# Kernel optimization log

Hardware: AMD Instinct MI355X
Metric: run time of the kernel (lower is better)

The kernel has to match this reference:

```python
import jax, jax.numpy as jnp
import numpy as np

CONV_CH, FRAG_DIM, N_P, N_T, PROJ = 32, 8, 6, 12, 64
B, T, W = 64, 256, 20


def _p(key, shape, scale=0.05):
    return (jax.random.normal(key, shape, dtype=jnp.float32) * scale)


def setup_inputs() -> dict:
    key = jax.random.key(0)
    ks = jax.random.split(key, 24)
    inp = {
        'pressure': jax.random.normal(ks[0], (B, T, W, N_P), dtype=jnp.float32),
        'torque': jax.random.normal(ks[1], (B, T, W, N_T), dtype=jnp.float32),
        'fragility': jax.random.uniform(ks[2], (B, 1), dtype=jnp.float32),
        # pressure encoder conv weights (O, I, K)
        'pw1': _p(ks[3], (CONV_CH, N_P, 3)), 'pb1': _p(ks[4], (CONV_CH,)),
        'pw2': _p(ks[5], (CONV_CH, CONV_CH, 3)), 'pb2': _p(ks[6], (CONV_CH,)),
        # torque encoder
        'tw1': _p(ks[7], (CONV_CH, N_T, 3)), 'tb1': _p(ks[8], (CONV_CH,)),
        'tw2': _p(ks[9], (CONV_CH, CONV_CH, 3)), 'tb2': _p(ks[10], (CONV_CH,)),
        # fragility Linear(1, 8)
        'fw': _p(ks[11], (FRAG_DIM, 1)), 'fb': _p(ks[12], (FRAG_DIM,)),
        # project Linear(72, 64)
        'prw': _p(ks[13], (PROJ, 2 * CONV_CH + FRAG_DIM)), 'prb': _p(ks[14], (PROJ,)),
        # LSTM (torch gate order i,f,g,o)
        'Wih': _p(ks[15], (4 * PROJ, PROJ)), 'Whh': _p(ks[16], (4 * PROJ, PROJ)),
        'bih': _p(ks[17], (4 * PROJ,)), 'bhh': _p(ks[18], (4 * PROJ,)),
        # head Linear(64, 4)
        'hw': _p(ks[19], (4, PROJ)), 'hb': _p(ks[20], (4,)),
    }
    return inp


def _conv1d(x, w, b):
    # x: (N, C, L), w: (O, I, K) -> (N, O, L-K+1), valid padding
    y = jax.lax.conv_general_dilated(x, w, (1,), 'VALID',
                                     dimension_numbers=('NCH', 'OIH', 'NCH'))
    return y + b[None, :, None]


def _encoder(x, w1, b1, w2, b2):
    # x: (N, C, L); conv-relu-conv-relu-global avg pool -> (N, CONV_CH)
    h = jax.nn.relu(_conv1d(x, w1, b1))
    h = jax.nn.relu(_conv1d(h, w2, b2))
    return jnp.mean(h, axis=-1)


def _lstm(x, Wih, Whh, bih, bhh):
    # x: (B, T, H); torch LSTM, gates i,f,g,o
    Bq, Tq, H = x.shape
    bias = bih + bhh
    xg = jnp.einsum('bth,gh->btg', x, Wih) + bias  # precompute input gates

    def step(carry, gt):
        h, c = carry
        g = gt + h @ Whh.T
        i, f, gg, o = jnp.split(g, 4, axis=-1)
        c = jax.nn.sigmoid(f) * c + jax.nn.sigmoid(i) * jnp.tanh(gg)
        h = jax.nn.sigmoid(o) * jnp.tanh(c)
        return (h, c), h

    init = (jnp.zeros((Bq, H), x.dtype), jnp.zeros((Bq, H), x.dtype))
    (hT, cT), hs = jax.lax.scan(step, init, xg.transpose(1, 0, 2))
    return hs.transpose(1, 0, 2), hT, cT


def reference(pressure, torque, fragility,
              pw1, pb1, pw2, pb2, tw1, tb1, tw2, tb2,
              fw, fb, prw, prb, Wih, Whh, bih, bhh, hw, hb):
    Bq, Tq = pressure.shape[:2]
    # batch all T windows at once: (B*T, C, L)
    p = pressure.reshape(Bq * Tq, W, N_P).transpose(0, 2, 1)
    t = torque.reshape(Bq * Tq, W, N_T).transpose(0, 2, 1)
    pf = _encoder(p, pw1, pb1, pw2, pb2)                    # (B*T, 32)
    tf = _encoder(t, tw1, tb1, tw2, tb2)                    # (B*T, 32)
    ff = jax.nn.relu(fragility @ fw.T + fb)                 # (B, 8)
    ff = jnp.broadcast_to(ff[:, None, :], (Bq, Tq, FRAG_DIM)).reshape(Bq * Tq, FRAG_DIM)
    cat = jnp.concatenate([pf, tf, ff], axis=1)             # (B*T, 72)
    feat = jax.nn.relu(cat @ prw.T + prb).reshape(Bq, Tq, PROJ)
    lstm_out, hT, cT = _lstm(feat, Wih, Whh, bih, bhh)
    out = jax.nn.sigmoid(lstm_out @ hw.T + hb)              # (B, T, 4)
    return out, hT, cT
```

## Files before the change

### kernel.cpp

```cpp
#include <hip/hip_runtime.h>
#include <math.h>

#define B_   64
#define T_   256
#define W_   20
#define NP_  6
#define NT_  12
#define CC_  32
#define FD_  8
#define PR_  64

#define LOG2E  1.4426950408889634f

typedef float v2f __attribute__((ext_vector_type(2)));
typedef _Float16 half2_t __attribute__((ext_vector_type(2)));

#define PINU(x) asm volatile("" : "+v"(x))
#define WAVE_SYNC() asm volatile("s_waitcnt lgkmcnt(0)" ::: "memory")

#define H2(u) __builtin_bit_cast(half2_t, (u))
#define EXP2N(x) __builtin_amdgcn_exp2f(x)


__device__ __forceinline__ unsigned packh2(float a, float b) {
    union { _Float16 h[2]; unsigned u; } cv;
    cv.h[0] = (_Float16)a; cv.h[1] = (_Float16)b;
    return cv.u;
}

__device__ __forceinline__ float sigmoidf_(float x) {
    return __builtin_amdgcn_rcpf(1.0f + EXP2N(-LOG2E * x));
}

#define W1PT_N  (18 * 64)
#define W2G_N   (64 * 48)
#define PRWT_N  (18 * 64 * 4)
#define WIHT_N  (16 * 4 * 64 * 4)
#define BSUM_N  256
#define PREP_TOTAL (W1PT_N + W2G_N + PRWT_N + WIHT_N + BSUM_N)

__global__ void prep_kernel(
    const float* __restrict__ pw1, const float* __restrict__ tw1,
    const float* __restrict__ pw2, const float* __restrict__ tw2,
    const float* __restrict__ prw, const float* __restrict__ Wih,
    const float* __restrict__ bih, const float* __restrict__ bhh,
    unsigned* __restrict__ w1pT, unsigned* __restrict__ w2g,
    float* __restrict__ prwT4, float* __restrict__ wihT4,
    float* __restrict__ bsum)
{
    int id = blockIdx.x * 256 + threadIdx.x;
    if (id < W1PT_N) {
        int lane = id & 63, m3 = id >> 6;
        int s = lane >> 5, o = lane & 31;
        int m = m3 / 3, k = m3 - 3 * m;
        unsigned v;
        if (s == 0)
            v = (m < 3) ? packh2(pw1[o * 18 + (2 * m) * 3 + k],
                                 pw1[o * 18 + (2 * m + 1) * 3 + k]) : 0u;
        else
            v = packh2(tw1[o * 36 + (2 * m) * 3 + k],
                       tw1[o * 36 + (2 * m + 1) * 3 + k]);
        w1pT[id] = v;
        return;
    }
    id -= W1PT_N;
    if (id < W2G_N) {
        int r = id / 48, c = id - 48 * r;
        int s = r >> 5, o = r & 31;
        int m = c / 3, k = c - 3 * m;
        const float* src = s ? tw2 : pw2;
        w2g[id] = packh2(src[o * 96 + (2 * m) * 3 + k],
                         src[o * 96 + (2 * m + 1) * 3 + k]);
        return;
    }
    id -= W2G_N;
    if (id < PRWT_N) {
        int j = id & 3, t = id >> 2;
        int lane = t & 63, kq = t >> 6;
        prwT4[id] = prw[lane * 72 + kq * 4 + j];
        return;
    }
    id -= PRWT_N;
    if (id < WIHT_N) {
        int j = id & 3, t = id >> 2;
        int lane = t & 63, gg = t >> 6;
        int gi = gg & 3, kq = gg >> 2;
        wihT4[id] = Wih[(gi * 64 + lane) * 64 + kq * 4 + j];
        return;
    }
    id -= WIHT_N;
    if (id < BSUM_N) bsum[id] = bih[id] + bhh[id];
}

__global__ __launch_bounds__(256, 4) void encoder_kernel(
    const float* __restrict__ pressure, const float* __restrict__ torque,
    const float* __restrict__ frag,
    const float* __restrict__ pb1, const float* __restrict__ tb1,
    const float* __restrict__ pb2, const float* __restrict__ tb2,
    const float* __restrict__ fw,  const float* __restrict__ fb,
    const float* __restrict__ prb,
    const unsigned* __restrict__ w1pT, const unsigned* __restrict__ w2g,
    const float* __restrict__ prwT4, const float* __restrict__ wihT4,
    const float* __restrict__ bsum,
    float* __restrict__ xg)
{
    const int tid  = threadIdx.x;
    const int wv   = tid >> 6;
    const int lane = tid & 63;
    const int bt   = blockIdx.x * 4 + wv;
    const int b    = bt >> 8;
    const int  o   = lane & 31;
    const bool isp = lane < 32;
    const int  s   = isp ? 0 : 1;

    __shared__ unsigned w2p[64 * 49];
    __shared__ __align__(16) unsigned xwp[4][2][120];
    __shared__ __align__(16) unsigned h1p[4][2][320];
    __shared__ __align__(16) float catb4[4][72];
    __shared__ __align__(16) float featsh4[4][64];

    float* catb   = catb4[wv];
    float* featsh = featsh4[wv];

    for (int idx = tid; idx < 64 * 48; idx += 256) {
        int r = idx / 48, c = idx - r * 48;
        w2p[r * 49 + c] = w2g[idx];
    }

    {
        unsigned* xz = &xwp[wv][0][0];
        #pragma unroll
        for (int idx = lane; idx < 240; idx += 64) xz[idx] = 0;
    }
    const float* pin = pressure + (size_t)bt * (W_ * NP_);
    for (int idx = lane; idx < W_ * NP_; idx += 64) {
        int w = idx / NP_, i = idx - w * NP_;
        ((_Float16*)&xwp[wv][0][(i >> 1) * 20 + w])[i & 1] = (_Float16)pin[idx];
    }
    const float* tin = torque + (size_t)bt * (W_ * NT_);
    for (int idx = lane; idx < W_ * NT_; idx += 64) {
        int w = idx / NT_, i = idx - w * NT_;
        ((_Float16*)&xwp[wv][1][(i >> 1) * 20 + w])[i & 1] = (_Float16)tin[idx];
    }
    if (lane < FD_) catb[64 + lane] = fmaxf(frag[b] * fw[lane] + fb[lane], 0.0f);

    unsigned w1p[18];
    #pragma unroll
    for (int m3 = 0; m3 < 18; ++m3) w1p[m3] = w1pT[m3 * 64 + lane];

    const float bz1 = isp ? pb1[o] : tb1[o];
    const float bz2 = isp ? pb2[o] : tb2[o];
    WAVE_SYNC();

    {
        const unsigned* xr = &xwp[wv][s][0];
        float acc[18];
        #pragma unroll
        for (int l = 0; l < 18; ++l) acc[l] = bz1;
        #pragma unroll
        for (int m = 0; m < 6; ++m) {
            uint4 r4[5];
            const uint4* rp = (const uint4*)(xr + m * 20);
            #pragma unroll
            for (int q = 0; q < 5; ++q) r4[q] = rp[q];
            const unsigned* rw = (const unsigned*)r4;
            const half2_t wk0 = H2(w1p[m * 3]), wk1 = H2(w1p[m * 3 + 1]), wk2 = H2(w1p[m * 3 + 2]);
            #pragma unroll
            for (int l = 0; l < 18; ++l) {
                float a = acc[l];
                a = __builtin_amdgcn_fdot2(wk0, H2(rw[l]),     a, false);
                a = __builtin_amdgcn_fdot2(wk1, H2(rw[l + 1]), a, false);
                a = __builtin_amdgcn_fdot2(wk2, H2(rw[l + 2]), a, false);
                acc[l] = a;
            }
        }
        #pragma unroll
        for (int l = 0; l < 18; ++l)
            ((_Float16*)&h1p[wv][s][(o >> 1) * 20 + l])[o & 1] = (_Float16)fmaxf(acc[l], 0.0f);
    }
    __syncthreads();

    {
        const unsigned* hr   = &h1p[wv][s][0];
        const unsigned* wrow = w2p + lane * 49;
        float sacc[16];
        #pragma unroll
        for (int l = 0; l < 16; ++l) sacc[l] = bz2;
        #pragma unroll 4
        for (int m = 0; m < 16; ++m) {
            uint4 r4[5];
            const uint4* rp = (const uint4*)(hr + m * 20);
            #pragma unroll
            for (int q = 0; q < 5; ++q) r4[q] = rp[q];
            const unsigned* rw = (const unsigned*)r4;
            const half2_t wk0 = H2(wrow[m * 3]), wk1 = H2(wrow[m * 3 + 1]), wk2 = H2(wrow[m * 3 + 2]);
            #pragma unroll
            for (int l = 0; l < 16; ++l) {
                float a = sacc[l];
                a = __builtin_amdgcn_fdot2(wk0, H2(rw[l]),     a, false);
                a = __builtin_amdgcn_fdot2(wk1, H2(rw[l + 1]), a, false);
                a = __builtin_amdgcn_fdot2(wk2, H2(rw[l + 2]), a, false);
                sacc[l] = a;
            }
        }
        float m2 = 0.0f;
        #pragma unroll
        for (int l = 0; l < 16; ++l) m2 += fmaxf(sacc[l], 0.0f);
        catb[lane] = m2 * 0.0625f;
    }
    WAVE_SYNC();

    {
        float acc = prb[lane];
        const float4* w4 = (const float4*)prwT4;
        const float4* c4 = (const float4*)catb;
        #pragma unroll
        for (int q = 0; q < 18; ++q) {
            float4 w = w4[q * 64 + lane];
            float4 cv = c4[q];
            acc += w.x * cv.x + w.y * cv.y + w.z * cv.z + w.w * cv.w;
        }
        featsh[lane] = fmaxf(acc, 0.0f);
    }
    WAVE_SYNC();

    {
        float4 fr[16];
        const float4* f4 = (const float4*)featsh;
        #pragma unroll
        for (int q = 0; q < 16; ++q) fr[q] = f4[q];
        float* xgrow = xg + (size_t)bt * 256;
        const float4* w44 = (const float4*)wihT4;
        #pragma unroll
        for (int gi = 0; gi < 4; ++gi) {
            float acc = bsum[gi * 64 + lane];
            #pragma unroll
            for (int q = 0; q < 16; ++q) {
                float4 w = w44[(q * 4 + gi) * 64 + lane];
                acc += w.x * fr[q].x + w.y * fr[q].y + w.z * fr[q].z + w.w * fr[q].w;
            }
            xgrow[gi * 64 + lane] = acc;
        }
    }
}

__global__ __launch_bounds__(64, 1) void lstm_kernel(
    const float* __restrict__ xg,
    const float* __restrict__ Whh,
    float* __restrict__ hout,
    float* __restrict__ dout)
{
    const int b = blockIdx.x;
    const int j = threadIdx.x;

    __shared__ __align__(16) _Float16 hs[64];

    unsigned wi[32], wf[32], wg[32], wo[32];
    {
        const v2f* ri = (const v2f*)(Whh + (size_t)(j)       * 64);
        const v2f* rf = (const v2f*)(Whh + (size_t)(64  + j) * 64);
        const v2f* rg = (const v2f*)(Whh + (size_t)(128 + j) * 64);
        const v2f* ro = (const v2f*)(Whh + (size_t)(192 + j) * 64);
        #pragma unroll
        for (int q = 0; q < 32; ++q) {
            v2f w;
            w = ri[q]; wi[q] = packh2(w.x, w.y);
            w = rf[q]; wf[q] = packh2(w.x, w.y);
            w = rg[q]; wg[q] = packh2(w.x, w.y);
            w = ro[q]; wo[q] = packh2(w.x, w.y);
        }
        #pragma unroll
        for (int q = 0; q < 32; ++q) { PINU(wi[q]); PINU(wf[q]); PINU(wg[q]); PINU(wo[q]); }
    }

    const float* xp = xg + (size_t)b * T_ * 256 + j;
    float4* hq4 = (float4*)(hout + (size_t)b * T_ * 64);

    float c = 0.0f;
    float h = 0.0f;
    hs[j] = (_Float16)0.0f;
    WAVE_SYNC();

    float xc0 = xp[0],   xc1 = xp[64],  xc2 = xp[128], xc3 = xp[192];
    float xn0 = xp[256], xn1 = xp[320], xn2 = xp[384], xn3 = xp[448];

    for (int tq = 0; tq < T_ / 4; ++tq) {
        float4 hacc;
        #pragma unroll
        for (int k = 0; k < 4; ++k) {
            const int t = tq * 4 + k;
            const int tp = (t + 2) * 256;
            float xf0 = xp[tp], xf1 = xp[tp + 64], xf2 = xp[tp + 128], xf3 = xp[tp + 192];

            uint4 hb[8];
            const uint4* hp = (const uint4*)hs;
            #pragma unroll
            for (int q = 0; q < 8; ++q) hb[q] = hp[q];
            const unsigned* hu = (const unsigned*)hb;

            float ai0 = xc0, af0 = xc1, ag0 = xc2, ao0 = xc3;
            float ai1 = 0.0f, af1 = 0.0f, ag1 = 0.0f, ao1 = 0.0f;
            #pragma unroll
            for (int q = 0; q < 32; q += 2) {
                half2_t h0 = H2(hu[q]), h1 = H2(hu[q + 1]);
                ai0 = __builtin_amdgcn_fdot2(H2(wi[q]),     h0, ai0, false);
                af0 = __builtin_amdgcn_fdot2(H2(wf[q]),     h0, af0, false);
                ag0 = __builtin_amdgcn_fdot2(H2(wg[q]),     h0, ag0, false);
                ao0 = __builtin_amdgcn_fdot2(H2(wo[q]),     h0, ao0, false);
                ai1 = __builtin_amdgcn_fdot2(H2(wi[q + 1]), h1, ai1, false);
                af1 = __builtin_amdgcn_fdot2(H2(wf[q + 1]), h1, af1, false);
                ag1 = __builtin_amdgcn_fdot2(H2(wg[q + 1]), h1, ag1, false);
                ao1 = __builtin_amdgcn_fdot2(H2(wo[q + 1]), h1, ao1, false);
            }
            const float ai = ai0 + ai1, af = af0 + af1;
            const float ag = ag0 + ag1, ao = ao0 + ao1;

            const float I = __builtin_amdgcn_rcpf(1.0f + EXP2N(-LOG2E * ai));
            const float F = __builtin_amdgcn_rcpf(1.0f + EXP2N(-LOG2E * af));
            const float O = __builtin_amdgcn_rcpf(1.0f + EXP2N(-LOG2E * ao));
            const float rgv = __builtin_amdgcn_rcpf(1.0f + EXP2N((2.0f * LOG2E) * ag));
            const float IG  = __builtin_fmaf(-(I + I), rgv, I);
            c = __builtin_fmaf(F, c, IG);
            const float rcv = __builtin_amdgcn_rcpf(1.0f + EXP2N((2.0f * LOG2E) * c));
            h = __builtin_fmaf(-(O + O), rcv, O);

            hs[j] = (_Float16)h;
            (&hacc.x)[k] = h;

            xc0 = xn0; xc1 = xn1; xc2 = xn2; xc3 = xn3;
            xn0 = xf0; xn1 = xf1; xn2 = xf2; xn3 = xf3;
        }
        hq4[tq * 64 + j] = hacc;
    }

    dout[B_ * T_ * 4 + b * 64 + j]           = h;
    dout[B_ * T_ * 4 + B_ * 64 + b * 64 + j] = c;
}

__global__ __launch_bounds__(256) void head_kernel(
    const float* __restrict__ hout, const float* __restrict__ hw,
    const float* __restrict__ hb, float* __restrict__ out)
{
    const int blk = blockIdx.x;
    const int tid = threadIdx.x;

    __shared__ __align__(16) float hsh[64 * 68];
    __shared__ __align__(16) float wsh[256];
    __shared__ float bsh[4];

    const float4* s4 = (const float4*)(hout + (size_t)blk * 64 * 64);
    for (int q = tid; q < 1024; q += 256) {
        int tqL = q >> 6;
        int j   = q & 63;
        float4 v = s4[q];
        #pragma unroll
        for (int k = 0; k < 4; ++k)
            hsh[(tqL * 4 + k) * 68 + j] = (&v.x)[k];
    }
    if (tid < 64) ((float4*)wsh)[tid] = ((const float4*)hw)[tid];
    if (tid < 4)  bsh[tid] = hb[tid];
    __syncthreads();

    const int r = tid >> 2, m = tid & 3;
    const float4* hv = (const float4*)(hsh + r * 68);
    const float4* wv = (const float4*)(wsh + m * 64);
    float acc = bsh[m];
    #pragma unroll
    for (int q = 0; q < 16; ++q) {
        float4 a = hv[q], w = wv[q];
        acc += a.x * w.x + a.y * w.y + a.z * w.z + a.w * w.w;
    }
    out[(size_t)blk * 256 + tid] = sigmoidf_(acc);
}

extern "C" void kernel_launch(void* const* d_in, const int* in_sizes, int n_in,
                              void* d_out, int out_size, void* d_ws, size_t ws_size,
                              hipStream_t stream) {
    const float* pressure = (const float*)d_in[0];
    const float* torque   = (const float*)d_in[1];
    const float* frag     = (const float*)d_in[2];
    const float* pw1 = (const float*)d_in[3];
    const float* pb1 = (const float*)d_in[4];
    const float* pw2 = (const float*)d_in[5];
    const float* pb2 = (const float*)d_in[6];
    const float* tw1 = (const float*)d_in[7];
    const float* tb1 = (const float*)d_in[8];
    const float* tw2 = (const float*)d_in[9];
    const float* tb2 = (const float*)d_in[10];
    const float* fw  = (const float*)d_in[11];
    const float* fb  = (const float*)d_in[12];
    const float* prw = (const float*)d_in[13];
    const float* prb = (const float*)d_in[14];
    const float* Wih = (const float*)d_in[15];
    const float* Whh = (const float*)d_in[16];
    const float* bih = (const float*)d_in[17];
    const float* bhh = (const float*)d_in[18];
    const float* hw  = (const float*)d_in[19];
    const float* hb  = (const float*)d_in[20];

    float* out = (float*)d_out;

    float* xg   = (float*)d_ws;
    float* hout = xg + (size_t)B_ * T_ * 256;

    unsigned* w1pT = (unsigned*)hout;
    unsigned* w2g  = w1pT + W1PT_N;
    float*   prwT4 = (float*)(w2g + W2G_N);
    float*   wihT4 = prwT4 + PRWT_N;
    float*   bsumP = wihT4 + WIHT_N;

    prep_kernel<<<(PREP_TOTAL + 255) / 256, 256, 0, stream>>>(
        pw1, tw1, pw2, tw2, prw, Wih, bih, bhh,
        w1pT, w2g, prwT4, wihT4, bsumP);

    encoder_kernel<<<B_ * T_ / 4, 256, 0, stream>>>(
        pressure, torque, frag,
        pb1, tb1, pb2, tb2, fw, fb, prb,
        w1pT, w2g, prwT4, wihT4, bsumP, xg);

    lstm_kernel<<<B_, 64, 0, stream>>>(xg, Whh, hout, out);

    head_kernel<<<B_ * T_ / 64, 256, 0, stream>>>(hout, hw, hb, out);
}
```

Baseline: 196.1 us.

## Fuse encoder and LSTM into one persistent kernel with per-chunk ready flags

```diff
diff --git a/kernel.cpp b/kernel.cpp
--- a/kernel.cpp
+++ b/kernel.cpp
@@ -39,15 +39,21 @@
 #define BSUM_N  256
 #define PREP_TOTAL (W1PT_N + W2G_N + PRWT_N + WIHT_N + BSUM_N)
 
+__device__ unsigned g_w1pT[W1PT_N];
+__device__ unsigned g_w2g[W2G_N];
+__device__ float    g_prwT4[PRWT_N];
+__device__ float    g_wihT4[WIHT_N];
+__device__ float    g_bsum[BSUM_N];
+__device__ unsigned long long g_ready[B_];
+
 __global__ void prep_kernel(
     const float* __restrict__ pw1, const float* __restrict__ tw1,
     const float* __restrict__ pw2, const float* __restrict__ tw2,
     const float* __restrict__ prw, const float* __restrict__ Wih,
-    const float* __restrict__ bih, const float* __restrict__ bhh,
-    unsigned* __restrict__ w1pT, unsigned* __restrict__ w2g,
-    float* __restrict__ prwT4, float* __restrict__ wihT4,
-    float* __restrict__ bsum)
+    const float* __restrict__ bih, const float* __restrict__ bhh)
 {
+    if (blockIdx.x == 0 && threadIdx.x < B_) g_ready[threadIdx.x] = 0ull;
+
     int id = blockIdx.x * 256 + threadIdx.x;
     if (id < W1PT_N) {
         int lane = id & 63, m3 = id >> 6;
@@ -60,7 +66,7 @@
         else
             v = packh2(tw1[o * 36 + (2 * m) * 3 + k],
                        tw1[o * 36 + (2 * m + 1) * 3 + k]);
-        w1pT[id] = v;
+        g_w1pT[id] = v;
         return;
     }
     id -= W1PT_N;
@@ -69,15 +75,15 @@
         int s = r >> 5, o = r & 31;
         int m = c / 3, k = c - 3 * m;
         const float* src = s ? tw2 : pw2;
-        w2g[id] = packh2(src[o * 96 + (2 * m) * 3 + k],
-                         src[o * 96 + (2 * m + 1) * 3 + k]);
+        g_w2g[id] = packh2(src[o * 96 + (2 * m) * 3 + k],
+                           src[o * 96 + (2 * m + 1) * 3 + k]);
         return;
     }
     id -= W2G_N;
     if (id < PRWT_N) {
         int j = id & 3, t = id >> 2;
         int lane = t & 63, kq = t >> 6;
-        prwT4[id] = prw[lane * 72 + kq * 4 + j];
+        g_prwT4[id] = prw[lane * 72 + kq * 4 + j];
         return;
     }
     id -= PRWT_N;
@@ -85,30 +91,143 @@
         int j = id & 3, t = id >> 2;
         int lane = t & 63, gg = t >> 6;
         int gi = gg & 3, kq = gg >> 2;
-        wihT4[id] = Wih[(gi * 64 + lane) * 64 + kq * 4 + j];
+        g_wihT4[id] = Wih[(gi * 64 + lane) * 64 + kq * 4 + j];
         return;
     }
     id -= WIHT_N;
-    if (id < BSUM_N) bsum[id] = bih[id] + bhh[id];
-}
-
-__global__ __launch_bounds__(256, 4) void encoder_kernel(
+    if (id < BSUM_N) g_bsum[id] = bih[id] + bhh[id];
+}
+
+__global__ __launch_bounds__(256, 2) void fused_kernel(
     const float* __restrict__ pressure, const float* __restrict__ torque,
     const float* __restrict__ frag,
     const float* __restrict__ pb1, const float* __restrict__ tb1,
     const float* __restrict__ pb2, const float* __restrict__ tb2,
     const float* __restrict__ fw,  const float* __restrict__ fb,
     const float* __restrict__ prb,
-    const unsigned* __restrict__ w1pT, const unsigned* __restrict__ w2g,
-    const float* __restrict__ prwT4, const float* __restrict__ wihT4,
-    const float* __restrict__ bsum,
-    float* __restrict__ xg)
+    const float* __restrict__ Whh,
+    float* __restrict__ xg,
+    float* __restrict__ hout,
+    float* __restrict__ dout)
 {
+    if (blockIdx.x < B_) {
+        if (threadIdx.x >= 64) return;
+        const int b = blockIdx.x;
+        const int j = threadIdx.x;
+
+        __shared__ __align__(16) _Float16 hs[64];
+
+        unsigned wi[32], wf[32], wg[32], wo[32];
+        {
+            const v2f* ri = (const v2f*)(Whh + (size_t)(j)       * 64);
+            const v2f* rf = (const v2f*)(Whh + (size_t)(64  + j) * 64);
+            const v2f* rg = (const v2f*)(Whh + (size_t)(128 + j) * 64);
+            const v2f* ro = (const v2f*)(Whh + (size_t)(192 + j) * 64);
+            #pragma unroll
+            for (int q = 0; q < 32; ++q) {
+                v2f w;
+                w = ri[q]; wi[q] = packh2(w.x, w.y);
+                w = rf[q]; wf[q] = packh2(w.x, w.y);
+                w = rg[q]; wg[q] = packh2(w.x, w.y);
+                w = ro[q]; wo[q] = packh2(w.x, w.y);
+            }
+            #pragma unroll
+            for (int q = 0; q < 32; ++q) { PINU(wi[q]); PINU(wf[q]); PINU(wg[q]); PINU(wo[q]); }
+        }
+        __builtin_amdgcn_s_setprio(1);
+
+        const float* xp = xg + (size_t)b * T_ * 256 + j;
+        float4* hq4 = (float4*)(hout + (size_t)b * T_ * 64);
+
+        float c = 0.0f;
+        float h = 0.0f;
+        hs[j] = (_Float16)0.0f;
+        WAVE_SYNC();
+
+        unsigned long long have = 0;
+        {
+            const unsigned long long m = 1ull;
+            while ((have & m) != m) {
+                have = __hip_atomic_load(&g_ready[b], __ATOMIC_ACQUIRE,
+                                         __HIP_MEMORY_SCOPE_AGENT);
+                if ((have & m) != m) __builtin_amdgcn_s_sleep(2);
+            }
+        }
+
+        float xc0 = xp[0],   xc1 = xp[64],  xc2 = xp[128], xc3 = xp[192];
+        float xn0 = xp[256], xn1 = xp[320], xn2 = xp[384], xn3 = xp[448];
+
+        for (int tq = 0; tq < T_ / 4; ++tq) {
+            {
+                const int ng = (tq + 2 > 64) ? 64 : tq + 2;
+                const unsigned long long m =
+                    (ng >= 64) ? ~0ull : ((1ull << ng) - 1ull);
+                while ((have & m) != m) {
+                    have = __hip_atomic_load(&g_ready[b], __ATOMIC_ACQUIRE,
+                                             __HIP_MEMORY_SCOPE_AGENT);
+                    if ((have & m) != m) __builtin_amdgcn_s_sleep(2);
+                }
+            }
+            float4 hacc;
+            #pragma unroll
+            for (int k = 0; k < 4; ++k) {
+                const int t = tq * 4 + k;
+                const int tp = (t + 2) * 256;
+                float xf0 = xp[tp], xf1 = xp[tp + 64], xf2 = xp[tp + 128], xf3 = xp[tp + 192];
+
+                uint4 hb[8];
+                const uint4* hp = (const uint4*)hs;
+                #pragma unroll
+                for (int q = 0; q < 8; ++q) hb[q] = hp[q];
+                const unsigned* hu = (const unsigned*)hb;
+
+                float ai0 = xc0, af0 = xc1, ag0 = xc2, ao0 = xc3;
+                float ai1 = 0.0f, af1 = 0.0f, ag1 = 0.0f, ao1 = 0.0f;
+                #pragma unroll
+                for (int q = 0; q < 32; q += 2) {
+                    half2_t h0 = H2(hu[q]), h1 = H2(hu[q + 1]);
+                    ai0 = __builtin_amdgcn_fdot2(H2(wi[q]),     h0, ai0, false);
+                    af0 = __builtin_amdgcn_fdot2(H2(wf[q]),     h0, af0, false);
+                    ag0 = __builtin_amdgcn_fdot2(H2(wg[q]),     h0, ag0, false);
+                    ao0 = __builtin_amdgcn_fdot2(H2(wo[q]),     h0, ao0, false);
+                    ai1 = __builtin_amdgcn_fdot2(H2(wi[q + 1]), h1, ai1, false);
+                    af1 = __builtin_amdgcn_fdot2(H2(wf[q + 1]), h1, af1, false);
+                    ag1 = __builtin_amdgcn_fdot2(H2(wg[q + 1]), h1, ag1, false);
+                    ao1 = __builtin_amdgcn_fdot2(H2(wo[q + 1]), h1, ao1, false);
+                }
+                const float ai = ai0 + ai1, af = af0 + af1;
+                const float ag = ag0 + ag1, ao = ao0 + ao1;
+
+                const float I = __builtin_amdgcn_rcpf(1.0f + EXP2N(-LOG2E * ai));
+                const float F = __builtin_amdgcn_rcpf(1.0f + EXP2N(-LOG2E * af));
+                const float O = __builtin_amdgcn_rcpf(1.0f + EXP2N(-LOG2E * ao));
+                const float rgv = __builtin_amdgcn_rcpf(1.0f + EXP2N((2.0f * LOG2E) * ag));
+                const float IG  = __builtin_fmaf(-(I + I), rgv, I);
+                c = __builtin_fmaf(F, c, IG);
+                const float rcv = __builtin_amdgcn_rcpf(1.0f + EXP2N((2.0f * LOG2E) * c));
+                h = __builtin_fmaf(-(O + O), rcv, O);
+
+                hs[j] = (_Float16)h;
+                (&hacc.x)[k] = h;
+
+                xc0 = xn0; xc1 = xn1; xc2 = xn2; xc3 = xn3;
+                xn0 = xf0; xn1 = xf1; xn2 = xf2; xn3 = xf3;
+            }
+            hq4[tq * 64 + j] = hacc;
+        }
+
+        dout[B_ * T_ * 4 + b * 64 + j]           = h;
+        dout[B_ * T_ * 4 + B_ * 64 + b * 64 + j] = c;
+        return;
+    }
+
+    const int eb   = blockIdx.x - B_;
     const int tid  = threadIdx.x;
     const int wv   = tid >> 6;
     const int lane = tid & 63;
-    const int bt   = blockIdx.x * 4 + wv;
-    const int b    = bt >> 8;
+    const int b    = eb & 63;
+    const int tg   = eb >> 6;
+    const int bt   = b * 256 + tg * 4 + wv;
     const int  o   = lane & 31;
     const bool isp = lane < 32;
     const int  s   = isp ? 0 : 1;
@@ -124,7 +243,7 @@
 
     for (int idx = tid; idx < 64 * 48; idx += 256) {
         int r = idx / 48, c = idx - r * 48;
-        w2p[r * 49 + c] = w2g[idx];
+        w2p[r * 49 + c] = g_w2g[idx];
     }
 
     {
@@ -146,7 +265,7 @@
 
     unsigned w1p[18];
     #pragma unroll
-    for (int m3 = 0; m3 < 18; ++m3) w1p[m3] = w1pT[m3 * 64 + lane];
+    for (int m3 = 0; m3 < 18; ++m3) w1p[m3] = g_w1pT[m3 * 64 + lane];
 
     const float bz1 = isp ? pb1[o] : tb1[o];
     const float bz2 = isp ? pb2[o] : tb2[o];
@@ -212,7 +331,7 @@
 
     {
         float acc = prb[lane];
-        const float4* w4 = (const float4*)prwT4;
+        const float4* w4 = (const float4*)g_prwT4;
         const float4* c4 = (const float4*)catb;
         #pragma unroll
         for (int q = 0; q < 18; ++q) {
@@ -230,10 +349,10 @@
         #pragma unroll
         for (int q = 0; q < 16; ++q) fr[q] = f4[q];
         float* xgrow = xg + (size_t)bt * 256;
-        const float4* w44 = (const float4*)wihT4;
+        const float4* w44 = (const float4*)g_wihT4;
         #pragma unroll
         for (int gi = 0; gi < 4; ++gi) {
-            float acc = bsum[gi * 64 + lane];
+            float acc = g_bsum[gi * 64 + lane];
             #pragma unroll
             for (int q = 0; q < 16; ++q) {
                 float4 w = w44[(q * 4 + gi) * 64 + lane];
@@ -242,99 +361,12 @@
             xgrow[gi * 64 + lane] = acc;
         }
     }
-}
-
-__global__ __launch_bounds__(64, 1) void lstm_kernel(
-    const float* __restrict__ xg,
-    const float* __restrict__ Whh,
-    float* __restrict__ hout,
-    float* __restrict__ dout)
-{
-    const int b = blockIdx.x;
-    const int j = threadIdx.x;
-
-    __shared__ __align__(16) _Float16 hs[64];
-
-    unsigned wi[32], wf[32], wg[32], wo[32];
-    {
-        const v2f* ri = (const v2f*)(Whh + (size_t)(j)       * 64);
-        const v2f* rf = (const v2f*)(Whh + (size_t)(64  + j) * 64);
-        const v2f* rg = (const v2f*)(Whh + (size_t)(128 + j) * 64);
-        const v2f* ro = (const v2f*)(Whh + (size_t)(192 + j) * 64);
-        #pragma unroll
-        for (int q = 0; q < 32; ++q) {
-            v2f w;
-            w = ri[q]; wi[q] = packh2(w.x, w.y);
-            w = rf[q]; wf[q] = packh2(w.x, w.y);
-            w = rg[q]; wg[q] = packh2(w.x, w.y);
-            w = ro[q]; wo[q] = packh2(w.x, w.y);
-        }
-        #pragma unroll
-        for (int q = 0; q < 32; ++q) { PINU(wi[q]); PINU(wf[q]); PINU(wg[q]); PINU(wo[q]); }
-    }
-
-    const float* xp = xg + (size_t)b * T_ * 256 + j;
-    float4* hq4 = (float4*)(hout + (size_t)b * T_ * 64);
-
-    float c = 0.0f;
-    float h = 0.0f;
-    hs[j] = (_Float16)0.0f;
-    WAVE_SYNC();
-
-    float xc0 = xp[0],   xc1 = xp[64],  xc2 = xp[128], xc3 = xp[192];
-    float xn0 = xp[256], xn1 = xp[320], xn2 = xp[384], xn3 = xp[448];
-
-    for (int tq = 0; tq < T_ / 4; ++tq) {
-        float4 hacc;
-        #pragma unroll
-        for (int k = 0; k < 4; ++k) {
-            const int t = tq * 4 + k;
-            const int tp = (t + 2) * 256;
-            float xf0 = xp[tp], xf1 = xp[tp + 64], xf2 = xp[tp + 128], xf3 = xp[tp + 192];
-
-            uint4 hb[8];
-            const uint4* hp = (const uint4*)hs;
-            #pragma unroll
-            for (int q = 0; q < 8; ++q) hb[q] = hp[q];
-            const unsigned* hu = (const unsigned*)hb;
-
-            float ai0 = xc0, af0 = xc1, ag0 = xc2, ao0 = xc3;
-            float ai1 = 0.0f, af1 = 0.0f, ag1 = 0.0f, ao1 = 0.0f;
-            #pragma unroll
-            for (int q = 0; q < 32; q += 2) {
-                half2_t h0 = H2(hu[q]), h1 = H2(hu[q + 1]);
-                ai0 = __builtin_amdgcn_fdot2(H2(wi[q]),     h0, ai0, false);
-                af0 = __builtin_amdgcn_fdot2(H2(wf[q]),     h0, af0, false);
-                ag0 = __builtin_amdgcn_fdot2(H2(wg[q]),     h0, ag0, false);
-                ao0 = __builtin_amdgcn_fdot2(H2(wo[q]),     h0, ao0, false);
-                ai1 = __builtin_amdgcn_fdot2(H2(wi[q + 1]), h1, ai1, false);
-                af1 = __builtin_amdgcn_fdot2(H2(wf[q + 1]), h1, af1, false);
-                ag1 = __builtin_amdgcn_fdot2(H2(wg[q + 1]), h1, ag1, false);
-                ao1 = __builtin_amdgcn_fdot2(H2(wo[q + 1]), h1, ao1, false);
-            }
-            const float ai = ai0 + ai1, af = af0 + af1;
-            const float ag = ag0 + ag1, ao = ao0 + ao1;
-
-            const float I = __builtin_amdgcn_rcpf(1.0f + EXP2N(-LOG2E * ai));
-            const float F = __builtin_amdgcn_rcpf(1.0f + EXP2N(-LOG2E * af));
-            const float O = __builtin_amdgcn_rcpf(1.0f + EXP2N(-LOG2E * ao));
-            const float rgv = __builtin_amdgcn_rcpf(1.0f + EXP2N((2.0f * LOG2E) * ag));
-            const float IG  = __builtin_fmaf(-(I + I), rgv, I);
-            c = __builtin_fmaf(F, c, IG);
-            const float rcv = __builtin_amdgcn_rcpf(1.0f + EXP2N((2.0f * LOG2E) * c));
-            h = __builtin_fmaf(-(O + O), rcv, O);
-
-            hs[j] = (_Float16)h;
-            (&hacc.x)[k] = h;
-
-            xc0 = xn0; xc1 = xn1; xc2 = xn2; xc3 = xn3;
-            xn0 = xf0; xn1 = xf1; xn2 = xf2; xn3 = xf3;
-        }
-        hq4[tq * 64 + j] = hacc;
-    }
-
-    dout[B_ * T_ * 4 + b * 64 + j]           = h;
-    dout[B_ * T_ * 4 + B_ * 64 + b * 64 + j] = c;
+
+    __syncthreads();
+    if (tid == 0) {
+        __threadfence();
+        atomicOr(&g_ready[b], 1ull << tg);
+    }
 }
 
 __global__ __launch_bounds__(256) void head_kernel(
@@ -403,22 +435,13 @@
     float* xg   = (float*)d_ws;
     float* hout = xg + (size_t)B_ * T_ * 256;
 
-    unsigned* w1pT = (unsigned*)hout;
-    unsigned* w2g  = w1pT + W1PT_N;
-    float*   prwT4 = (float*)(w2g + W2G_N);
-    float*   wihT4 = prwT4 + PRWT_N;
-    float*   bsumP = wihT4 + WIHT_N;
-
     prep_kernel<<<(PREP_TOTAL + 255) / 256, 256, 0, stream>>>(
-        pw1, tw1, pw2, tw2, prw, Wih, bih, bhh,
-        w1pT, w2g, prwT4, wihT4, bsumP);
-
-    encoder_kernel<<<B_ * T_ / 4, 256, 0, stream>>>(
+        pw1, tw1, pw2, tw2, prw, Wih, bih, bhh);
+
+    fused_kernel<<<B_ + B_ * T_ / 4, 256, 0, stream>>>(
         pressure, torque, frag,
         pb1, tb1, pb2, tb2, fw, fb, prb,
-        w1pT, w2g, prwT4, wihT4, bsumP, xg);
-
-    lstm_kernel<<<B_, 64, 0, stream>>>(xg, Whh, hout, out);
+        Whh, xg, hout, out);
 
     head_kernel<<<B_ * T_ / 64, 256, 0, stream>>>(hout, hw, hb, out);
 }
```

Measured after the change: 259.1 us. 32.1% more time.
